# Performance work log

Hardware: AMD Instinct MI355X
Metric: run time of the kernel (lower is better)

The kernel has to match this reference:

```python
import math
import jax, jax.numpy as jnp
import numpy as np

N, L, D = 64, 128, 768          # batch, n_in capsules, feature dim
IN_DIM, OUT_DIM, N_OUT = 64, 64, 32
EPS = 1e-8

def _xavier(k, shape):
    # torch xavier_uniform: fan_in = shape[1]*prod(shape[2:]), fan_out = shape[0]*prod(shape[2:])
    rec = int(np.prod(shape[2:])) if len(shape) > 2 else 1
    fan_in, fan_out = shape[-2] * rec, shape[-1] * rec
    a = math.sqrt(6.0 / (fan_in + fan_out))
    return jax.random.uniform(k, shape, jnp.float32, -a, a)

def setup_inputs() -> dict:
    key = jax.random.key(0)
    ks = jax.random.split(key, 4)
    return {
        "x": jax.random.normal(ks[0], (N, L, D), jnp.float32),
        "Wscore": _xavier(ks[1], (L, D, 1)),
        "Bscore": jnp.zeros((L, 1, 1), jnp.float32),
        "Wcap": _xavier(ks[2], (L, D, IN_DIM)),
        "Bcap": jnp.zeros((L, 1, IN_DIM), jnp.float32),
        "Wvote": _xavier(ks[3], (L, N_OUT, IN_DIM, OUT_DIM)),
        "Bvote": jnp.zeros((L, N_OUT, 1, OUT_DIM), jnp.float32),
        "beta_use": jnp.zeros((L, 1, 1, 1), jnp.float32),
        "beta_ign": jnp.zeros((1, N_OUT, 1, 1), jnp.float32),
        "iters": 3,
    }

def reference(x, Wscore, Bscore, Wcap, Bcap, Wvote, Bvote, beta_use, beta_ign, iters):
    n_out = Wvote.shape[1]
    pi = jnp.asarray(math.pi, x.dtype)
    x_t = jnp.transpose(x, (1, 0, 2))                     # (L, N, D)
    a_in = jnp.matmul(x_t, Wscore) + Bscore               # (L, N, 1)
    mu_in = jax.nn.gelu(jnp.matmul(x_t, Wcap) + Bcap, approximate=False)  # (L, N, in_dim)
    f_a_in = jax.nn.sigmoid(a_in)[:, None, :, :]          # (L, 1, N, 1)
    # votes: (L, n_out, N, out_dim)
    V = jnp.einsum('lni,loij->lonj', mu_in, Wvote) + Bvote

    def em_step(R):
        D_use = f_a_in * R                                # (L, n_out, N, 1)
        D_ign = f_a_in - D_use
        a_out = jnp.sum(beta_use * D_use, axis=0) - jnp.sum(beta_ign * D_ign, axis=0)  # (n_out, N, 1)
        denom = jnp.sum(D_use, axis=0) + EPS              # (n_out, N, 1)
        mu_out = jnp.sum(D_use * V, axis=0) / denom       # (n_out, N, out_dim)
        var_out = jnp.sum(D_use * (V - mu_out[None]) ** 2, axis=0) / denom
        return a_out, mu_out, var_out

    R = jnp.full((1, n_out, 1, 1), 1.0 / n_out, dtype=x.dtype)
    a_out, mu_out, var_out = em_step(R)
    for _ in range(int(iters) - 1):
        # Gaussian log-likelihood of each vote under each output capsule
        log_p = (-jnp.sum((V - mu_out[None]) ** 2 / (2.0 * var_out[None] + EPS), axis=-1)
                 - 1.0 - 0.5 * pi
                 - 0.5 * jnp.sum(jnp.log(var_out[None] + EPS), axis=-1))   # (L, n_out, N)
        R = jax.nn.softmax(jax.nn.log_sigmoid(a_out)[None] + log_p[..., None], axis=1)
        a_out, mu_out, var_out = em_step(R)

    a_out = jnp.transpose(a_out[..., 0], (1, 0))          # (N, n_out)
    mu_out = jnp.transpose(mu_out, (1, 0, 2))             # (N, n_out, out_dim)
    return a_out, mu_out
```

## Files before the change

### kernel.cpp

```cpp
#include <hip/hip_runtime.h>
#include <math.h>

#define NB 64
#define LL 128
#define DD 768
#define ID 64
#define OD 64
#define NO 32
#define EPSF 1e-8f

typedef unsigned short ushort_t;
typedef __attribute__((ext_vector_type(8))) short bf16x8;
typedef __attribute__((ext_vector_type(4))) float f32x4;


__device__ __forceinline__ float gelu_exact(float v) {
  return 0.5f * v * (1.0f + erff(v * 0.70710678118654752440f));
}
__device__ __forceinline__ float sigmoidf_(float z) {
  return 1.0f / (1.0f + __expf(-z));
}
__device__ __forceinline__ unsigned short f2bf(float f) {
  unsigned u = __float_as_uint(f);
  unsigned r = (u + 0x7FFFu + ((u >> 16) & 1u)) >> 16;
  return (unsigned short)r;
}
__device__ __forceinline__ float bf2f(unsigned short s) {
  return __uint_as_float(((unsigned)s) << 16);
}

__global__ __launch_bounds__(256) void k0a_proj(
    const float* __restrict__ x, const float* __restrict__ Wscore,
    const float* __restrict__ Wcap,
    float* __restrict__ Cpart, float* __restrict__ apart)
{
  const int l  = blockIdx.x & 127;
  const int kc = blockIdx.x >> 7;
  const int t = threadIdx.x;
  const int tn = t >> 4;
  const int ti = t & 15;
  __shared__ float Xs[64][68];
  __shared__ float Ws[64][68];
  __shared__ float Ss[64];
  float C[4][4] = {{0.f}};
  float asum[4] = {0.f, 0.f, 0.f, 0.f};

  for (int kt = 0; kt < 2; ++kt) {
    const int kbase = kc * 128 + kt * 64;
#pragma unroll
    for (int r = 0; r < 4; ++r) {
      const int flat = r * 1024 + t * 4;
      const int p = flat >> 6, qq = flat & 63;
      *(float4*)&Xs[p][qq] = *(const float4*)&x[(p * LL + l) * DD + kbase + qq];
      *(float4*)&Ws[p][qq] = *(const float4*)&Wcap[(l * DD + kbase + p) * ID + qq];
    }
    if (t < 16)
      *(float4*)&Ss[4 * t] = *(const float4*)&Wscore[l * DD + kbase + 4 * t];
    __syncthreads();
#pragma unroll 8
    for (int k = 0; k < 64; ++k) {
      float av[4];
      av[0] = Xs[4 * tn + 0][k];
      av[1] = Xs[4 * tn + 1][k];
      av[2] = Xs[4 * tn + 2][k];
      av[3] = Xs[4 * tn + 3][k];
      const float4 b = *(const float4*)&Ws[k][4 * ti];
      const float sk = Ss[k];
#pragma unroll
      for (int a = 0; a < 4; ++a) {
        C[a][0] = fmaf(av[a], b.x, C[a][0]);
        C[a][1] = fmaf(av[a], b.y, C[a][1]);
        C[a][2] = fmaf(av[a], b.z, C[a][2]);
        C[a][3] = fmaf(av[a], b.w, C[a][3]);
        asum[a] = fmaf(av[a], sk, asum[a]);
      }
    }
    __syncthreads();
  }
#pragma unroll
  for (int a = 0; a < 4; ++a)
    *(float4*)&Cpart[kc * 524288 + (l * 64 + 4 * tn + a) * 64 + 4 * ti] =
        make_float4(C[a][0], C[a][1], C[a][2], C[a][3]);
  if (ti == 0) {
#pragma unroll
    for (int a = 0; a < 4; ++a)
      apart[kc * 8192 + l * 64 + 4 * tn + a] = asum[a];
  }
}

__global__ __launch_bounds__(256) void k0bc(
    const float* __restrict__ Cpart, const float* __restrict__ Bcap,
    const float* __restrict__ apart, const float* __restrict__ Bscore,
    ushort_t* __restrict__ Ah, ushort_t* __restrict__ Al,
    float* __restrict__ f_a)
{
  const int bid = blockIdx.x;
  const int t = threadIdx.x;
  const int e = (bid * 256 + t) * 4;
  float4 s = *(const float4*)&Cpart[e];
#pragma unroll
  for (int kc = 1; kc < 6; ++kc) {
    const float4 p = *(const float4*)&Cpart[kc * 524288 + e];
    s.x += p.x; s.y += p.y; s.z += p.z; s.w += p.w;
  }
  const int l = e >> 12;
  const int n = (e >> 6) & 63;
  const int i0 = e & 63;
  const float4 bc = *(const float4*)&Bcap[l * 64 + i0];
  float m[4] = {gelu_exact(s.x + bc.x), gelu_exact(s.y + bc.y),
                gelu_exact(s.z + bc.z), gelu_exact(s.w + bc.w)};
  ushort4 h, lo;
  h.x = f2bf(m[0]); lo.x = f2bf(m[0] - bf2f(h.x));
  h.y = f2bf(m[1]); lo.y = f2bf(m[1] - bf2f(h.y));
  h.z = f2bf(m[2]); lo.z = f2bf(m[2] - bf2f(h.z));
  h.w = f2bf(m[3]); lo.w = f2bf(m[3] - bf2f(h.w));
  const int off = l * 4096 + (i0 >> 5) * 2048 + (n >> 4) * 512 + (n & 15) * 32 +
                  ((i0 >> 3) & 3) * 8 + (i0 & 7);
  *(ushort4*)&Ah[off] = h;
  *(ushort4*)&Al[off] = lo;

  if (bid < 32) {
    const int e2 = bid * 256 + t;
    float ss = 0.f;
#pragma unroll
    for (int kc = 0; kc < 6; ++kc) ss += apart[kc * 8192 + e2];
    f_a[e2] = sigmoidf_(ss + Bscore[e2 >> 6]);
  }
}

__global__ __launch_bounds__(256) void k1_votes(
    const ushort_t* __restrict__ Ah, const ushort_t* __restrict__ Al,
    const float* __restrict__ Wvote, const float* __restrict__ Bvote,
    float* __restrict__ V)
{
  const int t = threadIdx.x;
  const int w = t >> 6;
  const int lane = t & 63;
  const int g = blockIdx.x * 4 + w;
  const int pair = g >> 1;
  const int jh = g & 1;
  const int l = pair >> 5;
  const int mr = lane & 15, q = lane >> 4;

  __shared__ unsigned HL_all[4][1024];
  unsigned* HL = HL_all[w];

  const float* Wt = Wvote + (size_t)pair * 4096 + jh * 32;
  const int afoff = mr * 32 + q * 8;

  float bv[2];
#pragma unroll
  for (int nt = 0; nt < 2; ++nt)
    bv[nt] = Bvote[pair * 64 + jh * 32 + 16 * nt + mr];

  f32x4 acc[4][2];
#pragma unroll
  for (int mt = 0; mt < 4; ++mt)
#pragma unroll
    for (int nt = 0; nt < 2; ++nt) {
      f32x4 z = {0.f, 0.f, 0.f, 0.f};
      acc[mt][nt] = z;
    }

#pragma unroll 1
  for (int ks = 0; ks < 2; ++ks) {
#pragma unroll
    for (int f = 0; f < 4; ++f) {
      const int idx = f * 64 + lane;
      const int r = idx >> 3;
      const int c4 = (idx & 7) * 4;
      const float4 v4 = *(const float4*)&Wt[ks * 2048 + r * 64 + c4];
      const int jc = c4 ^ ((r & 8) << 1);
      const float e4[4] = {v4.x, v4.y, v4.z, v4.w};
      unsigned pk[4];
#pragma unroll
      for (int d = 0; d < 4; ++d) {
        const unsigned short hi = f2bf(e4[d]);
        const unsigned short lo = f2bf(e4[d] - bf2f(hi));
        pk[d] = (unsigned)hi | ((unsigned)lo << 16);
      }
      *(uint4*)&HL[r * 32 + jc] = make_uint4(pk[0], pk[1], pk[2], pk[3]);
    }

    bf16x8 afh[4], afl[4];
#pragma unroll
    for (int mt = 0; mt < 4; ++mt) {
      const int off = l * 4096 + ks * 2048 + mt * 512 + afoff;
      afh[mt] = *(const bf16x8*)&Ah[off];
      afl[mt] = *(const bf16x8*)&Al[off];
    }

#pragma unroll
    for (int nt = 0; nt < 2; ++nt) {
      const int j = 16 * nt + mr;
      unsigned wv[8];
#pragma unroll
      for (int d = 0; d < 8; ++d) {
        const int ii = q * 8 + d;
        wv[d] = HL[ii * 32 + (j ^ ((ii & 8) << 1))];
      }
      union { ushort_t u[8]; bf16x8 v; } bh, bl;
#pragma unroll
      for (int d = 0; d < 8; ++d) {
        bh.u[d] = (ushort_t)(wv[d] & 0xffffu);
        bl.u[d] = (ushort_t)(wv[d] >> 16);
      }
#pragma unroll
      for (int mt = 0; mt < 4; ++mt) {
        acc[mt][nt] = __builtin_amdgcn_mfma_f32_16x16x32_bf16(
            afh[mt], bh.v, acc[mt][nt], 0, 0, 0);
        acc[mt][nt] = __builtin_amdgcn_mfma_f32_16x16x32_bf16(
            afh[mt], bl.v, acc[mt][nt], 0, 0, 0);
        acc[mt][nt] = __builtin_amdgcn_mfma_f32_16x16x32_bf16(
            afl[mt], bh.v, acc[mt][nt], 0, 0, 0);
      }
    }
  }

  float* T = (float*)HL;
#pragma unroll
  for (int mt = 0; mt < 4; ++mt) {
#pragma unroll
    for (int nt = 0; nt < 2; ++nt)
#pragma unroll
      for (int r = 0; r < 4; ++r)
        T[(4 * q + r) * 36 + 16 * nt + mr] = acc[mt][nt][r] + bv[nt];
#pragma unroll
    for (int rr = 0; rr < 2; ++rr) {
      const int row = rr * 8 + (lane >> 3);
      const int c4e = (lane & 7) * 4;
      const float4 vv = *(const float4*)&T[row * 36 + c4e];
      const size_t base = (size_t)(16 * mt + row) * (LL * NO * OD) +
                          (size_t)pair * 64 + jh * 32 + c4e;
      *(float4*)&V[base] = vv;
    }
  }
}

__global__ __launch_bounds__(256) void k3u_em(
    const float* __restrict__ V, const float* __restrict__ f_a,
    const float* __restrict__ beta_use,
    float* __restrict__ S1p, float* __restrict__ S2p,
    float* __restrict__ dnp, float* __restrict__ aUp)
{
  const int n  = blockIdx.x >> 4;
  const int c  = (blockIdx.x >> 1) & 7;
  const int jh = blockIdx.x & 1;
  const int t = threadIdx.x;
  const int o = t >> 3, q = t & 7;
  const int j0 = jh * 32 + q * 4;

  float aS1[4] = {0.f, 0.f, 0.f, 0.f};
  float aS2[4] = {0.f, 0.f, 0.f, 0.f};
  float dn = 0.f, aU = 0.f;

  const float* Vb = V + (size_t)n * LL * 2048 + o * 64 + j0;
#pragma unroll
  for (int u = 0; u < 16; ++u) {
    const int l = c * 16 + u;
    const float4 v = *(const float4*)&Vb[(size_t)l * 2048];
    const float wgt = f_a[l * NB + n] * (1.0f / NO);
    dn += wgt;
    aU = fmaf(beta_use[l], wgt, aU);
    aS1[0] = fmaf(wgt, v.x, aS1[0]);
    aS1[1] = fmaf(wgt, v.y, aS1[1]);
    aS1[2] = fmaf(wgt, v.z, aS1[2]);
    aS1[3] = fmaf(wgt, v.w, aS1[3]);
    aS2[0] = fmaf(wgt * v.x, v.x, aS2[0]);
    aS2[1] = fmaf(wgt * v.y, v.y, aS2[1]);
    aS2[2] = fmaf(wgt * v.z, v.z, aS2[2]);
    aS2[3] = fmaf(wgt * v.w, v.w, aS2[3]);
  }

  const int base = ((c * NB + n) * NO + o) * OD + j0;
  *(float4*)&S1p[base] = make_float4(aS1[0], aS1[1], aS1[2], aS1[3]);
  *(float4*)&S2p[base] = make_float4(aS2[0], aS2[1], aS2[2], aS2[3]);
  if (q == 0 && jh == 0) {
    dnp[(c * NB + n) * NO + o] = dn;
    aUp[(c * NB + n) * NO + o] = aU;
  }
}

__global__ __launch_bounds__(256) void k3_em(
    const float* __restrict__ V, const float* __restrict__ f_a,
    const float* __restrict__ beta_use, const float* __restrict__ mu_s,
    const float* __restrict__ i2v_s, const float* __restrict__ cterm,
    float* __restrict__ S1p, float* __restrict__ S2p,
    float* __restrict__ dnp, float* __restrict__ aUp, const int mode)
{
  const int n = blockIdx.x >> 3;
  const int c = blockIdx.x & 7;
  const int t = threadIdx.x;
  const int o = t >> 3, q = t & 7;
  __shared__ float ttl[8][32];

  float mu8[8], iv8[8];
  float ct = 0.f;
  if (mode) {
    const float4 a0 = *(const float4*)&mu_s[n * 2048 + t * 8];
    const float4 a1 = *(const float4*)&mu_s[n * 2048 + t * 8 + 4];
    mu8[0] = a0.x; mu8[1] = a0.y; mu8[2] = a0.z; mu8[3] = a0.w;
    mu8[4] = a1.x; mu8[5] = a1.y; mu8[6] = a1.z; mu8[7] = a1.w;
    const float4 b0 = *(const float4*)&i2v_s[n * 2048 + t * 8];
    const float4 b1 = *(const float4*)&i2v_s[n * 2048 + t * 8 + 4];
    iv8[0] = b0.x; iv8[1] = b0.y; iv8[2] = b0.z; iv8[3] = b0.w;
    iv8[4] = b1.x; iv8[5] = b1.y; iv8[6] = b1.z; iv8[7] = b1.w;
    ct = cterm[n * NO + o];
  }
  float aS1[8] = {0.f, 0.f, 0.f, 0.f, 0.f, 0.f, 0.f, 0.f};
  float aS2[8] = {0.f, 0.f, 0.f, 0.f, 0.f, 0.f, 0.f, 0.f};
  float dn = 0.f, aU = 0.f;

  const float* Vb = V + (size_t)n * LL * 2048 + t * 8;

  float VA[4][8], VB[4][8], faA[4], faB[4], buA[4], buB[4];

  auto LOAD = [&](float (&Vv)[4][8], float (&fa4)[4], float (&bu4)[4],
                  const int g) {
    const int lb = c * 16 + g * 4;
#pragma unroll
    for (int u = 0; u < 4; ++u) {
      const int l = lb + u;
      const float4 v0 = *(const float4*)&Vb[(size_t)l * 2048];
      const float4 v1 = *(const float4*)&Vb[(size_t)l * 2048 + 4];
      Vv[u][0] = v0.x; Vv[u][1] = v0.y; Vv[u][2] = v0.z; Vv[u][3] = v0.w;
      Vv[u][4] = v1.x; Vv[u][5] = v1.y; Vv[u][6] = v1.z; Vv[u][7] = v1.w;
      fa4[u] = f_a[l * NB + n];
      bu4[u] = beta_use[l];
    }
  };

  auto COMP = [&](float (&Vv)[4][8], float (&fa4)[4], float (&bu4)[4],
                  const int g) {
    if (mode) {
      float tt4[4];
#pragma unroll
      for (int u = 0; u < 4; ++u) {
        float s2 = 0.f;
#pragma unroll
        for (int k = 0; k < 8; ++k) {
          const float d = Vv[u][k] - mu8[k];
          s2 = fmaf(d * d, iv8[k], s2);
        }
        s2 += __shfl_xor(s2, 1);
        s2 += __shfl_xor(s2, 2);
        s2 += __shfl_xor(s2, 4);
        tt4[u] = ct - s2;
      }
      const int sb = (g & 1) * 4;
      if (q == 0) {
#pragma unroll
        for (int u = 0; u < 4; ++u) ttl[sb + u][o] = tt4[u];
      }
      __syncthreads();
#pragma unroll
      for (int u = 0; u < 4; ++u) {
        const float vv = ttl[sb + u][t & 31];
        float m = vv;
#pragma unroll
        for (int msk = 1; msk <= 16; msk <<= 1) m = fmaxf(m, __shfl_xor(m, msk));
        float z = __expf(vv - m);
#pragma unroll
        for (int msk = 1; msk <= 16; msk <<= 1) z += __shfl_xor(z, msk);
        const float wgt = fa4[u] * __expf(tt4[u] - m) / z;
        dn += wgt;
        aU = fmaf(bu4[u], wgt, aU);
#pragma unroll
        for (int k = 0; k < 8; ++k) {
          const float d = Vv[u][k] - mu8[k];
          aS1[k] = fmaf(wgt, Vv[u][k], aS1[k]);
          aS2[k] = fmaf(wgt, d * d, aS2[k]);
        }
      }
    } else {
#pragma unroll
      for (int u = 0; u < 4; ++u) {
        const float wgt = fa4[u] * (1.0f / NO);
        dn += wgt;
        aU = fmaf(bu4[u], wgt, aU);
#pragma unroll
        for (int k = 0; k < 8; ++k) {
          aS1[k] = fmaf(wgt, Vv[u][k], aS1[k]);
          aS2[k] = fmaf(wgt * Vv[u][k], Vv[u][k], aS2[k]);
        }
      }
    }
  };

  LOAD(VA, faA, buA, 0);
  LOAD(VB, faB, buB, 1);
  COMP(VA, faA, buA, 0);
  LOAD(VA, faA, buA, 2);
  COMP(VB, faB, buB, 1);
  LOAD(VB, faB, buB, 3);
  COMP(VA, faA, buA, 2);
  COMP(VB, faB, buB, 3);

  const int base = ((c * NB + n) * NO + o) * OD + q * 8;
  *(float4*)&S1p[base]     = make_float4(aS1[0], aS1[1], aS1[2], aS1[3]);
  *(float4*)&S1p[base + 4] = make_float4(aS1[4], aS1[5], aS1[6], aS1[7]);
  if (mode != 2) {
    *(float4*)&S2p[base]     = make_float4(aS2[0], aS2[1], aS2[2], aS2[3]);
    *(float4*)&S2p[base + 4] = make_float4(aS2[4], aS2[5], aS2[6], aS2[7]);
  }
  if (q == 0) {
    dnp[(c * NB + n) * NO + o] = dn;
    aUp[(c * NB + n) * NO + o] = aU;
  }
}

__global__ __launch_bounds__(64) void k4_fin23(
    const float* __restrict__ S1p, const float* __restrict__ S2p,
    const float* __restrict__ dnp, const float* __restrict__ aUp,
    const float* __restrict__ f_a, const float* __restrict__ beta_ign,
    float* __restrict__ mu_s, float* __restrict__ i2v_s, float* __restrict__ cterm,
    float* __restrict__ out, const int final_iter, const int first)
{
  const int n = blockIdx.x >> 5;
  const int o = blockIdx.x & 31;
  const int j = threadIdx.x;

  float fs = f_a[j * NB + n] + f_a[(j + 64) * NB + n];
#pragma unroll
  for (int msk = 32; msk >= 1; msk >>= 1) fs += __shfl_xor(fs, msk);
  const float Fsum = fs;

  float dn = 0.f, aU = 0.f;
#pragma unroll
  for (int cc = 0; cc < 8; ++cc) {
    dn += dnp[(cc * NB + n) * NO + o];
    aU += aUp[(cc * NB + n) * NO + o];
  }
  const float S0 = dn;
  const float inv_den = 1.0f / (dn + EPSF);

  float S1 = 0.f;
#pragma unroll
  for (int cc = 0; cc < 8; ++cc)
    S1 += S1p[((cc * NB + n) * NO + o) * OD + j];

  const float aout = aU - beta_ign[o] * (Fsum - dn);
  const float mu = S1 * inv_den;

  if (final_iter) {
    if (j == 0) out[n * NO + o] = aout;
    out[2048 + n * 2048 + o * 64 + j] = mu;
  } else {
    float S2 = 0.f;
#pragma unroll
    for (int cc = 0; cc < 8; ++cc)
      S2 += S2p[((cc * NB + n) * NO + o) * OD + j];
    const float mup = first ? 0.f : mu_s[n * 2048 + o * 64 + j];
    const float dd = mu - mup;
    const float varn = S2 - 2.0f * dd * (S1 - mup * S0) + dd * dd * S0;
    const float var = fmaxf(varn * inv_den, 0.0f);
    mu_s[n * 2048 + o * 64 + j] = mu;
    i2v_s[n * 2048 + o * 64 + j] = 1.0f / (2.0f * var + EPSF);
    float lacc = logf(var + EPSF);
#pragma unroll
    for (int msk = 32; msk >= 1; msk >>= 1) lacc += __shfl_xor(lacc, msk);
    if (j == 0) {
      const float lsg = fminf(aout, 0.0f) - log1pf(__expf(-fabsf(aout)));
      cterm[n * NO + o] = lsg - 0.5f * lacc;
    }
  }
}

extern "C" void kernel_launch(void* const* d_in, const int* in_sizes, int n_in,
                              void* d_out, int out_size, void* d_ws, size_t ws_size,
                              hipStream_t stream) {
  const float* x        = (const float*)d_in[0];
  const float* Wscore   = (const float*)d_in[1];
  const float* Bscore   = (const float*)d_in[2];
  const float* Wcap     = (const float*)d_in[3];
  const float* Bcap     = (const float*)d_in[4];
  const float* Wvote    = (const float*)d_in[5];
  const float* Bvote    = (const float*)d_in[6];
  const float* beta_use = (const float*)d_in[7];
  const float* beta_ign = (const float*)d_in[8];
  float* out = (float*)d_out;

  float* ws     = (float*)d_ws;
  float* V      = ws;
  float* Cpart  = ws;
  float* apart  = ws + 3145728;
  ushort_t* Ah  = (ushort_t*)(ws + 16777216);
  ushort_t* Al  = Ah + 524288;
  float* f_a    = ws + 16777216 + 524288;
  float* S1p    = f_a + 8192;
  float* S2p    = S1p + 1048576;
  float* dnp    = S2p + 1048576;
  float* aUp    = dnp + 16384;
  float* mu_s   = aUp + 16384;
  float* i2v_s  = mu_s + 131072;
  float* ct     = i2v_s + 131072;
  const size_t need = (size_t)(16777216 + 524288 + 8192 + 2 * 1048576 +
                               2 * 16384 + 2 * 131072 + 2048) * sizeof(float);
  if (ws_size < need) return;

  k0a_proj<<<768, 256, 0, stream>>>(x, Wscore, Wcap, Cpart, apart);
  k0bc<<<512, 256, 0, stream>>>(Cpart, Bcap, apart, Bscore, Ah, Al, f_a);
  k1_votes<<<2048, 256, 0, stream>>>(Ah, Al, Wvote, Bvote, V);
  k3u_em<<<1024, 256, 0, stream>>>(V, f_a, beta_use, S1p, S2p, dnp, aUp);
  k4_fin23<<<2048, 64, 0, stream>>>(S1p, S2p, dnp, aUp, f_a, beta_ign, mu_s, i2v_s, ct, out, 0, 1);
  k3_em<<<512, 256, 0, stream>>>(V, f_a, beta_use, mu_s, i2v_s, ct, S1p, S2p, dnp, aUp, 1);
  k4_fin23<<<2048, 64, 0, stream>>>(S1p, S2p, dnp, aUp, f_a, beta_ign, mu_s, i2v_s, ct, out, 0, 0);
  k3_em<<<512, 256, 0, stream>>>(V, f_a, beta_use, mu_s, i2v_s, ct, S1p, S2p, dnp, aUp, 2);
  k4_fin23<<<2048, 64, 0, stream>>>(S1p, S2p, dnp, aUp, f_a, beta_ign, mu_s, i2v_s, ct, out, 1, 0);
}
```

Measured before the change: 241.9 us.

## Restructure EM routing kernel to wave-per-chunk with LDS transpose and 16-way L split

Replaces the block-wide EM routing kernel with a wave-per-(n, L-chunk) design. Each lane owns one output capsule and a half of its 64 dims, so the log-likelihood reduction and the softmax over output capsules become intra-wave shuffles instead of needing a __syncthreads and shared-memory exchange. V rows are staged through padded LDS to transpose them into per-lane layout, and the partial sums are written back the same way. The L dimension is split into 16 chunks instead of 8, which doubles the partial buffers and the reduction work in the finalize kernel. The trade-off is more work in the finalize step and higher register pressure, since each lane holds 32-wide mu, inverse-variance and accumulator arrays.

```diff
diff --git a/kernel.cpp b/kernel.cpp
--- a/kernel.cpp
+++ b/kernel.cpp
@@ -243,8 +243,8 @@
     float* __restrict__ S1p, float* __restrict__ S2p,
     float* __restrict__ dnp, float* __restrict__ aUp)
 {
-  const int n  = blockIdx.x >> 4;
-  const int c  = (blockIdx.x >> 1) & 7;
+  const int n  = blockIdx.x >> 5;
+  const int c  = (blockIdx.x >> 1) & 15;
   const int jh = blockIdx.x & 1;
   const int t = threadIdx.x;
   const int o = t >> 3, q = t & 7;
@@ -256,8 +256,8 @@
 
   const float* Vb = V + (size_t)n * LL * 2048 + o * 64 + j0;
 #pragma unroll
-  for (int u = 0; u < 16; ++u) {
-    const int l = c * 16 + u;
+  for (int u = 0; u < 8; ++u) {
+    const int l = c * 8 + u;
     const float4 v = *(const float4*)&Vb[(size_t)l * 2048];
     const float wgt = f_a[l * NB + n] * (1.0f / NO);
     dn += wgt;
@@ -281,129 +281,116 @@
   }
 }
 
-__global__ __launch_bounds__(256) void k3_em(
+__global__ __launch_bounds__(256) void k3w_em(
     const float* __restrict__ V, const float* __restrict__ f_a,
     const float* __restrict__ beta_use, const float* __restrict__ mu_s,
     const float* __restrict__ i2v_s, const float* __restrict__ cterm,
     float* __restrict__ S1p, float* __restrict__ S2p,
     float* __restrict__ dnp, float* __restrict__ aUp, const int mode)
 {
-  const int n = blockIdx.x >> 3;
-  const int c = blockIdx.x & 7;
   const int t = threadIdx.x;
-  const int o = t >> 3, q = t & 7;
-  __shared__ float ttl[8][32];
-
-  float mu8[8], iv8[8];
-  float ct = 0.f;
-  if (mode) {
-    const float4 a0 = *(const float4*)&mu_s[n * 2048 + t * 8];
-    const float4 a1 = *(const float4*)&mu_s[n * 2048 + t * 8 + 4];
-    mu8[0] = a0.x; mu8[1] = a0.y; mu8[2] = a0.z; mu8[3] = a0.w;
-    mu8[4] = a1.x; mu8[5] = a1.y; mu8[6] = a1.z; mu8[7] = a1.w;
-    const float4 b0 = *(const float4*)&i2v_s[n * 2048 + t * 8];
-    const float4 b1 = *(const float4*)&i2v_s[n * 2048 + t * 8 + 4];
-    iv8[0] = b0.x; iv8[1] = b0.y; iv8[2] = b0.z; iv8[3] = b0.w;
-    iv8[4] = b1.x; iv8[5] = b1.y; iv8[6] = b1.z; iv8[7] = b1.w;
-    ct = cterm[n * NO + o];
-  }
-  float aS1[8] = {0.f, 0.f, 0.f, 0.f, 0.f, 0.f, 0.f, 0.f};
-  float aS2[8] = {0.f, 0.f, 0.f, 0.f, 0.f, 0.f, 0.f, 0.f};
+  const int w = t >> 6;
+  const int lane = t & 63;
+  const int W = blockIdx.x * 4 + w;
+  const int n = W >> 4;
+  const int c = W & 15;
+  const int o = lane & 31;
+  const int jh = lane >> 5;
+
+  __shared__ float STG[4][2][2176];
+
+  float mu[32], iv[32];
+  const int mib = n * 2048 + o * 64 + jh * 32;
+#pragma unroll
+  for (int kk = 0; kk < 8; ++kk) {
+    const float4 a = *(const float4*)&mu_s[mib + kk * 4];
+    mu[kk*4+0] = a.x; mu[kk*4+1] = a.y; mu[kk*4+2] = a.z; mu[kk*4+3] = a.w;
+    const float4 b = *(const float4*)&i2v_s[mib + kk * 4];
+    iv[kk*4+0] = b.x; iv[kk*4+1] = b.y; iv[kk*4+2] = b.z; iv[kk*4+3] = b.w;
+  }
+  const float ct = cterm[n * NO + o];
+
+  float aS1[32], aS2[32];
+#pragma unroll
+  for (int k = 0; k < 32; ++k) { aS1[k] = 0.f; aS2[k] = 0.f; }
   float dn = 0.f, aU = 0.f;
 
-  const float* Vb = V + (size_t)n * LL * 2048 + t * 8;
-
-  float VA[4][8], VB[4][8], faA[4], faB[4], buA[4], buB[4];
-
-  auto LOAD = [&](float (&Vv)[4][8], float (&fa4)[4], float (&bu4)[4],
-                  const int g) {
-    const int lb = c * 16 + g * 4;
-#pragma unroll
-    for (int u = 0; u < 4; ++u) {
-      const int l = lb + u;
-      const float4 v0 = *(const float4*)&Vb[(size_t)l * 2048];
-      const float4 v1 = *(const float4*)&Vb[(size_t)l * 2048 + 4];
-      Vv[u][0] = v0.x; Vv[u][1] = v0.y; Vv[u][2] = v0.z; Vv[u][3] = v0.w;
-      Vv[u][4] = v1.x; Vv[u][5] = v1.y; Vv[u][6] = v1.z; Vv[u][7] = v1.w;
-      fa4[u] = f_a[l * NB + n];
-      bu4[u] = beta_use[l];
-    }
-  };
-
-  auto COMP = [&](float (&Vv)[4][8], float (&fa4)[4], float (&bu4)[4],
-                  const int g) {
-    if (mode) {
-      float tt4[4];
-#pragma unroll
-      for (int u = 0; u < 4; ++u) {
-        float s2 = 0.f;
-#pragma unroll
-        for (int k = 0; k < 8; ++k) {
-          const float d = Vv[u][k] - mu8[k];
-          s2 = fmaf(d * d, iv8[k], s2);
-        }
-        s2 += __shfl_xor(s2, 1);
-        s2 += __shfl_xor(s2, 2);
-        s2 += __shfl_xor(s2, 4);
-        tt4[u] = ct - s2;
-      }
-      const int sb = (g & 1) * 4;
-      if (q == 0) {
-#pragma unroll
-        for (int u = 0; u < 4; ++u) ttl[sb + u][o] = tt4[u];
-      }
-      __syncthreads();
-#pragma unroll
-      for (int u = 0; u < 4; ++u) {
-        const float vv = ttl[sb + u][t & 31];
-        float m = vv;
-#pragma unroll
-        for (int msk = 1; msk <= 16; msk <<= 1) m = fmaxf(m, __shfl_xor(m, msk));
-        float z = __expf(vv - m);
-#pragma unroll
-        for (int msk = 1; msk <= 16; msk <<= 1) z += __shfl_xor(z, msk);
-        const float wgt = fa4[u] * __expf(tt4[u] - m) / z;
-        dn += wgt;
-        aU = fmaf(bu4[u], wgt, aU);
-#pragma unroll
-        for (int k = 0; k < 8; ++k) {
-          const float d = Vv[u][k] - mu8[k];
-          aS1[k] = fmaf(wgt, Vv[u][k], aS1[k]);
-          aS2[k] = fmaf(wgt, d * d, aS2[k]);
-        }
+  const int rT = lane >> 4;
+  const int cT = (lane & 15) * 4;
+
+#pragma unroll 1
+  for (int u = 0; u < 8; ++u) {
+    const int l = c * 8 + u;
+    float* T = STG[w][u & 1];
+    const float* Vr = V + ((size_t)n * LL + l) * 2048;
+#pragma unroll
+    for (int f = 0; f < 8; ++f) {
+      const float4 v4 = *(const float4*)&Vr[f * 256 + lane * 4];
+      *(float4*)&T[(f * 4 + rT) * 68 + cT] = v4;
+    }
+    float v[32];
+#pragma unroll
+    for (int kk = 0; kk < 8; ++kk) {
+      const float4 r4 = *(const float4*)&T[o * 68 + jh * 32 + kk * 4];
+      v[kk*4+0] = r4.x; v[kk*4+1] = r4.y; v[kk*4+2] = r4.z; v[kk*4+3] = r4.w;
+    }
+    float s2 = 0.f;
+#pragma unroll
+    for (int k = 0; k < 32; ++k) {
+      const float d = v[k] - mu[k];
+      s2 = fmaf(d * d, iv[k], s2);
+    }
+    s2 += __shfl_xor(s2, 32);
+    const float tt = ct - s2;
+    float m = tt;
+#pragma unroll
+    for (int msk = 1; msk <= 16; msk <<= 1) m = fmaxf(m, __shfl_xor(m, msk));
+    float z = __expf(tt - m);
+#pragma unroll
+    for (int msk = 1; msk <= 16; msk <<= 1) z += __shfl_xor(z, msk);
+    const float wgt = f_a[l * NB + n] * __expf(tt - m) / z;
+    dn += wgt;
+    aU = fmaf(beta_use[l], wgt, aU);
+    if (mode != 2) {
+#pragma unroll
+      for (int k = 0; k < 32; ++k) {
+        aS1[k] = fmaf(wgt, v[k], aS1[k]);
+        const float d = v[k] - mu[k];
+        aS2[k] = fmaf(wgt, d * d, aS2[k]);
       }
     } else {
 #pragma unroll
-      for (int u = 0; u < 4; ++u) {
-        const float wgt = fa4[u] * (1.0f / NO);
-        dn += wgt;
-        aU = fmaf(bu4[u], wgt, aU);
-#pragma unroll
-        for (int k = 0; k < 8; ++k) {
-          aS1[k] = fmaf(wgt, Vv[u][k], aS1[k]);
-          aS2[k] = fmaf(wgt * Vv[u][k], Vv[u][k], aS2[k]);
-        }
-      }
-    }
-  };
-
-  LOAD(VA, faA, buA, 0);
-  LOAD(VB, faB, buB, 1);
-  COMP(VA, faA, buA, 0);
-  LOAD(VA, faA, buA, 2);
-  COMP(VB, faB, buB, 1);
-  LOAD(VB, faB, buB, 3);
-  COMP(VA, faA, buA, 2);
-  COMP(VB, faB, buB, 3);
-
-  const int base = ((c * NB + n) * NO + o) * OD + q * 8;
-  *(float4*)&S1p[base]     = make_float4(aS1[0], aS1[1], aS1[2], aS1[3]);
-  *(float4*)&S1p[base + 4] = make_float4(aS1[4], aS1[5], aS1[6], aS1[7]);
+      for (int k = 0; k < 32; ++k)
+        aS1[k] = fmaf(wgt, v[k], aS1[k]);
+    }
+  }
+
+  const size_t cb = (size_t)(c * NB + n) * 2048;
+  {
+    float* T = STG[w][0];
+#pragma unroll
+    for (int kk = 0; kk < 8; ++kk)
+      *(float4*)&T[o * 68 + jh * 32 + kk * 4] =
+          make_float4(aS1[kk*4+0], aS1[kk*4+1], aS1[kk*4+2], aS1[kk*4+3]);
+#pragma unroll
+    for (int f = 0; f < 8; ++f) {
+      const float4 r4 = *(const float4*)&T[(f * 4 + rT) * 68 + cT];
+      *(float4*)&S1p[cb + f * 256 + lane * 4] = r4;
+    }
+  }
   if (mode != 2) {
-    *(float4*)&S2p[base]     = make_float4(aS2[0], aS2[1], aS2[2], aS2[3]);
-    *(float4*)&S2p[base + 4] = make_float4(aS2[4], aS2[5], aS2[6], aS2[7]);
-  }
-  if (q == 0) {
+    float* T = STG[w][1];
+#pragma unroll
+    for (int kk = 0; kk < 8; ++kk)
+      *(float4*)&T[o * 68 + jh * 32 + kk * 4] =
+          make_float4(aS2[kk*4+0], aS2[kk*4+1], aS2[kk*4+2], aS2[kk*4+3]);
+#pragma unroll
+    for (int f = 0; f < 8; ++f) {
+      const float4 r4 = *(const float4*)&T[(f * 4 + rT) * 68 + cT];
+      *(float4*)&S2p[cb + f * 256 + lane * 4] = r4;
+    }
+  }
+  if (jh == 0) {
     dnp[(c * NB + n) * NO + o] = dn;
     aUp[(c * NB + n) * NO + o] = aU;
   }
@@ -427,7 +414,7 @@
 
   float dn = 0.f, aU = 0.f;
 #pragma unroll
-  for (int cc = 0; cc < 8; ++cc) {
+  for (int cc = 0; cc < 16; ++cc) {
     dn += dnp[(cc * NB + n) * NO + o];
     aU += aUp[(cc * NB + n) * NO + o];
   }
@@ -436,7 +423,7 @@
 
   float S1 = 0.f;
 #pragma unroll
-  for (int cc = 0; cc < 8; ++cc)
+  for (int cc = 0; cc < 16; ++cc)
     S1 += S1p[((cc * NB + n) * NO + o) * OD + j];
 
   const float aout = aU - beta_ign[o] * (Fsum - dn);
@@ -448,7 +435,7 @@
   } else {
     float S2 = 0.f;
 #pragma unroll
-    for (int cc = 0; cc < 8; ++cc)
+    for (int cc = 0; cc < 16; ++cc)
       S2 += S2p[((cc * NB + n) * NO + o) * OD + j];
     const float mup = first ? 0.f : mu_s[n * 2048 + o * 64 + j];
     const float dd = mu - mup;
@@ -488,23 +475,23 @@
   ushort_t* Al  = Ah + 524288;
   float* f_a    = ws + 16777216 + 524288;
   float* S1p    = f_a + 8192;
-  float* S2p    = S1p + 1048576;
-  float* dnp    = S2p + 1048576;
-  float* aUp    = dnp + 16384;
-  float* mu_s   = aUp + 16384;
+  float* S2p    = S1p + 2097152;
+  float* dnp    = S2p + 2097152;
+  float* aUp    = dnp + 32768;
+  float* mu_s   = aUp + 32768;
   float* i2v_s  = mu_s + 131072;
   float* ct     = i2v_s + 131072;
-  const size_t need = (size_t)(16777216 + 524288 + 8192 + 2 * 1048576 +
-                               2 * 16384 + 2 * 131072 + 2048) * sizeof(float);
+  const size_t need = (size_t)(16777216 + 524288 + 8192 + 2 * 2097152 +
+                               2 * 32768 + 2 * 131072 + 2048) * sizeof(float);
   if (ws_size < need) return;
 
   k0a_proj<<<768, 256, 0, stream>>>(x, Wscore, Wcap, Cpart, apart);
   k0bc<<<512, 256, 0, stream>>>(Cpart, Bcap, apart, Bscore, Ah, Al, f_a);
   k1_votes<<<2048, 256, 0, stream>>>(Ah, Al, Wvote, Bvote, V);
-  k3u_em<<<1024, 256, 0, stream>>>(V, f_a, beta_use, S1p, S2p, dnp, aUp);
+  k3u_em<<<2048, 256, 0, stream>>>(V, f_a, beta_use, S1p, S2p, dnp, aUp);
   k4_fin23<<<2048, 64, 0, stream>>>(S1p, S2p, dnp, aUp, f_a, beta_ign, mu_s, i2v_s, ct, out, 0, 1);
-  k3_em<<<512, 256, 0, stream>>>(V, f_a, beta_use, mu_s, i2v_s, ct, S1p, S2p, dnp, aUp, 1);
+  k3w_em<<<256, 256, 0, stream>>>(V, f_a, beta_use, mu_s, i2v_s, ct, S1p, S2p, dnp, aUp, 1);
   k4_fin23<<<2048, 64, 0, stream>>>(S1p, S2p, dnp, aUp, f_a, beta_ign, mu_s, i2v_s, ct, out, 0, 0);
-  k3_em<<<512, 256, 0, stream>>>(V, f_a, beta_use, mu_s, i2v_s, ct, S1p, S2p, dnp, aUp, 2);
+  k3w_em<<<256, 256, 0, stream>>>(V, f_a, beta_use, mu_s, i2v_s, ct, S1p, S2p, dnp, aUp, 2);
   k4_fin23<<<2048, 64, 0, stream>>>(S1p, S2p, dnp, aUp, f_a, beta_ign, mu_s, i2v_s, ct, out, 1, 0);
 }
```

After: 250.8 us. 1.04x slower.
